# Kernel tuning notes

Hardware: AMD Instinct MI355X
Metric: run time of the kernel (lower is better)

## Reference

```python
import jax, jax.numpy as jnp
import numpy as np

N_NODES = 50000
N_EDGES = 800000
D = 128
N_LAYERS = 5
N_REL = 500
N_ENT = 50000  # fc output size (num_entities)
BATCH = 1024


def setup_inputs() -> dict:
    key = jax.random.key(0)
    ks = jax.random.split(key, 10)
    return {
        "entity_embed": jax.random.normal(ks[0], (N_NODES, D), dtype=jnp.float32),
        "edge_val": jnp.ones((N_EDGES,), dtype=jnp.float32),
        "gnn_W": jax.random.normal(ks[1], (N_LAYERS, D, D), dtype=jnp.float32) * (1.0 / np.sqrt(D)),
        "gnn_b": jax.random.normal(ks[2], (N_LAYERS, D), dtype=jnp.float32) * 0.01,
        "rel_table": jax.random.normal(ks[3], (N_REL, D), dtype=jnp.float32),
        "fc_W": jax.random.normal(ks[4], (2 * D, N_ENT), dtype=jnp.float32) * (1.0 / np.sqrt(2 * D)),
        "fc_b": jax.random.normal(ks[5], (N_ENT,), dtype=jnp.float32) * 0.01,
        "edge_row": jax.random.randint(ks[6], (N_EDGES,), 0, N_NODES, dtype=jnp.int32),
        "edge_col": jax.random.randint(ks[7], (N_EDGES,), 0, N_NODES, dtype=jnp.int32),
        "head_idx": jax.random.randint(ks[8], (BATCH,), 0, N_NODES, dtype=jnp.int32),
        "rel_ids": jax.random.randint(ks[9], (BATCH,), 0, N_REL, dtype=jnp.int32),
    }


def reference(entity_embed, edge_val, gnn_W, gnn_b, rel_table, fc_W, fc_b,
              edge_row, edge_col, head_idx, rel_ids):
    n_nodes = entity_embed.shape[0]

    def layer(x, wb):
        W, b = wb
        # sparse.mm(adj, x): out[row] += val * x[col]
        msgs = edge_val[:, None] * x[edge_col]          # [E, D]
        agg = jax.ops.segment_sum(msgs, edge_row, num_segments=n_nodes)  # [N, D]
        return jax.nn.relu(agg @ W + b), None

    all_embed, _ = jax.lax.scan(layer, entity_embed, (gnn_W, gnn_b))

    head_embed = all_embed[head_idx]                    # [B, D]
    rel_embed = rel_table[rel_ids]                      # [B, D]
    embed = jnp.concatenate([head_embed, rel_embed], axis=1)  # [B, 2D]
    logits = embed @ fc_W + fc_b                        # [B, N_ENT]
    return logits
```

## Files before the change

kernel.cpp:

```cpp
#include <hip/hip_runtime.h>


#define N_NODES 50000
#define N_EDGES 800000
#define D 128
#define N_LAYERS 5
#define N_ENT 50000
#define BATCH 1024
#define KDIM 256
#define SCAN_BLOCKS ((N_NODES + 255) / 256)
#define FC_NT 128

typedef __attribute__((ext_vector_type(8))) __bf16 bf16x8;
typedef __attribute__((ext_vector_type(4))) float f32x4;
typedef __attribute__((ext_vector_type(8))) unsigned short u16x8;
typedef __attribute__((ext_vector_type(4))) unsigned short u16x4;

__device__ inline unsigned short f2bf(float x) {
  unsigned int u = __float_as_uint(x);
  unsigned int r = (u + 0x7FFFu + ((u >> 16) & 1u)) >> 16;
  return (unsigned short)r;
}
__device__ inline float bf2f(unsigned short b) {
  return __uint_as_float(((unsigned int)b) << 16);
}

__global__ void zero_i32(int* __restrict__ p, int n) {
  int i = blockIdx.x * blockDim.x + threadIdx.x;
  if (i < n) p[i] = 0;
}

__global__ void hist_kernel(const int* __restrict__ rows, int* __restrict__ counts) {
  int i = blockIdx.x * blockDim.x + threadIdx.x;
  int stride = gridDim.x * blockDim.x;
  for (; i < N_EDGES; i += stride) atomicAdd(&counts[rows[i]], 1);
}

__device__ inline int block_exscan256(int v, int* wsum, int* tot) {
  int t = threadIdx.x, lane = t & 63, wid = t >> 6;
  int s = v;
#pragma unroll
  for (int off = 1; off < 64; off <<= 1) {
    int u = __shfl_up(s, off, 64);
    if (lane >= off) s += u;
  }
  if (lane == 63) wsum[wid] = s;
  __syncthreads();
  if (t == 0) {
    int run = 0;
#pragma unroll
    for (int w = 0; w < 4; ++w) { int tmp = wsum[w]; wsum[w] = run; run += tmp; }
    wsum[4] = run;
  }
  __syncthreads();
  *tot = wsum[4];
  return wsum[wid] + s - v;
}

__global__ __launch_bounds__(256) void scan1_kernel(const int* __restrict__ counts,
                                                    int* __restrict__ row_ptr,
                                                    int* __restrict__ bsum) {
  __shared__ int wsum[5];
  int i = blockIdx.x * 256 + threadIdx.x;
  int v = (i < N_NODES) ? counts[i] : 0;
  int tot;
  int ex = block_exscan256(v, wsum, &tot);
  if (i < N_NODES) row_ptr[i] = ex;
  if (threadIdx.x == 0) bsum[blockIdx.x] = tot;
}

__global__ __launch_bounds__(256) void scan2_kernel(int* __restrict__ bsum) {
  __shared__ int wsum[5];
  int t = threadIdx.x;
  int v = (t < SCAN_BLOCKS) ? bsum[t] : 0;
  int tot;
  int ex = block_exscan256(v, wsum, &tot);
  if (t < SCAN_BLOCKS) bsum[t] = ex;
}

__global__ __launch_bounds__(256) void scan3_kernel(const int* __restrict__ counts,
                                                    const int* __restrict__ bsum,
                                                    int* __restrict__ row_ptr,
                                                    int* __restrict__ cursor) {
  int i = blockIdx.x * 256 + threadIdx.x;
  if (i >= N_NODES) return;
  int ex = row_ptr[i] + bsum[blockIdx.x];
  row_ptr[i] = ex;
  cursor[i] = ex;
  if (i == N_NODES - 1) row_ptr[N_NODES] = ex + counts[i];
}

__global__ void scatter_kernel(const int* __restrict__ rows, const int* __restrict__ cols,
                               const float* __restrict__ vals, int* __restrict__ cursor,
                               int* __restrict__ col_s, float* __restrict__ val_s) {
  int i = blockIdx.x * blockDim.x + threadIdx.x;
  int stride = gridDim.x * blockDim.x;
  for (; i < N_EDGES; i += stride) {
    int r = rows[i];
    int pos = atomicAdd(&cursor[r], 1);
    col_s[pos] = cols[i];
    val_s[pos] = vals[i];
  }
}

__global__ __launch_bounds__(256) void tobf16_kernel(const float* __restrict__ src,
                                                     unsigned short* __restrict__ dst,
                                                     int n8) {
  int i = blockIdx.x * blockDim.x + threadIdx.x;
  if (i >= n8) return;
  float4 a = *(const float4*)&src[i * 8];
  float4 b = *(const float4*)&src[i * 8 + 4];
  u16x8 o;
  o[0] = f2bf(a.x); o[1] = f2bf(a.y); o[2] = f2bf(a.z); o[3] = f2bf(a.w);
  o[4] = f2bf(b.x); o[5] = f2bf(b.y); o[6] = f2bf(b.z); o[7] = f2bf(b.w);
  *(u16x8*)&dst[i * 8] = o;
}

__global__ void wconv_kernel(const float* __restrict__ gW, unsigned short* __restrict__ Wt5) {
  int idx = blockIdx.x * 256 + threadIdx.x;
  if (idx >= N_LAYERS * D * D) return;
  int l = idx / (D * D);
  int rem = idx - l * D * D;
  int j = rem >> 7;
  int k = rem & 127;
  Wt5[idx] = f2bf(gW[l * D * D + k * D + j]);
}

__global__ __launch_bounds__(256) void layer_fused(const unsigned short* __restrict__ xb,
                                                   const int* __restrict__ row_ptr,
                                                   const int* __restrict__ cols,
                                                   const float* __restrict__ vals,
                                                   const unsigned short* __restrict__ Bt,
                                                   const float* __restrict__ bias,
                                                   unsigned short* __restrict__ yb) {
  __shared__ unsigned short atile[64 * D];
  int t = threadIdx.x, lane = t & 63, wave = t >> 6;
  int q = lane >> 4, l16 = lane & 15;
  int r0 = blockIdx.x * 64;
  char* ab = (char*)atile;

#pragma unroll
  for (int p = 0; p < 4; ++p) {
    int row_l = wave * 16 + p * 4 + q;
    int r = r0 + row_l;
    float acc[8] = {0.f, 0.f, 0.f, 0.f, 0.f, 0.f, 0.f, 0.f};
    if (r < N_NODES) {
      int e0 = row_ptr[r], e1 = row_ptr[r + 1];
      for (int base = e0; base < e1; base += 16) {
        int idx = base + l16;
        bool ok = idx < e1;
        int cl = ok ? cols[idx] : 0;
        float vl = ok ? vals[idx] : 0.f;
        int cnt = min(16, e1 - base);
        int j = 0;
        for (; j + 4 <= cnt; j += 4) {
          int c[4]; float v[4]; u16x8 xv[4];
#pragma unroll
          for (int u = 0; u < 4; ++u) {
            c[u] = __shfl(cl, q * 16 + j + u);
            v[u] = __shfl(vl, q * 16 + j + u);
          }
#pragma unroll
          for (int u = 0; u < 4; ++u) xv[u] = *(const u16x8*)&xb[c[u] * D + l16 * 8];
#pragma unroll
          for (int u = 0; u < 4; ++u)
#pragma unroll
            for (int dd = 0; dd < 8; ++dd) acc[dd] = fmaf(v[u], bf2f(xv[u][dd]), acc[dd]);
        }
        for (; j < cnt; ++j) {
          int c = __shfl(cl, q * 16 + j);
          float v = __shfl(vl, q * 16 + j);
          u16x8 xv0 = *(const u16x8*)&xb[c * D + l16 * 8];
#pragma unroll
          for (int dd = 0; dd < 8; ++dd) acc[dd] = fmaf(v, bf2f(xv0[dd]), acc[dd]);
        }
      }
    }
    u16x8 o;
#pragma unroll
    for (int dd = 0; dd < 8; ++dd) o[dd] = f2bf(acc[dd]);
    *(u16x8*)(ab + row_l * 256 + ((l16 ^ (row_l & 7)) << 4)) = o;
  }
  __syncthreads();

  int lq = lane >> 4;
  f32x4 acc2[4][2];
#pragma unroll
  for (int m = 0; m < 4; ++m) { acc2[m][0] = (f32x4){0,0,0,0}; acc2[m][1] = (f32x4){0,0,0,0}; }
#pragma unroll
  for (int kk = 0; kk < 4; ++kk) {
    bf16x8 wfr[2];
#pragma unroll
    for (int nt = 0; nt < 2; ++nt)
      wfr[nt] = *(const bf16x8*)&Bt[(wave * 32 + nt * 16 + l16) * D + kk * 32 + lq * 8];
#pragma unroll
    for (int m = 0; m < 4; ++m) {
      int row_l = m * 16 + l16;
      bf16x8 afr = *(const bf16x8*)(ab + row_l * 256 + ((((kk * 4 + lq) ^ (row_l & 7)) << 4)));
      acc2[m][0] = __builtin_amdgcn_mfma_f32_16x16x32_bf16(wfr[0], afr, acc2[m][0], 0, 0, 0);
      acc2[m][1] = __builtin_amdgcn_mfma_f32_16x16x32_bf16(wfr[1], afr, acc2[m][1], 0, 0, 0);
    }
  }
#pragma unroll
  for (int nt = 0; nt < 2; ++nt) {
    int jb = wave * 32 + nt * 16 + lq * 4;
    float4 bb = *(const float4*)&bias[jb];
#pragma unroll
    for (int m = 0; m < 4; ++m) {
      int r = r0 + m * 16 + l16;
      if (r < N_NODES) {
        u16x4 o;
        o[0] = f2bf(fmaxf(acc2[m][nt][0] + bb.x, 0.f));
        o[1] = f2bf(fmaxf(acc2[m][nt][1] + bb.y, 0.f));
        o[2] = f2bf(fmaxf(acc2[m][nt][2] + bb.z, 0.f));
        o[3] = f2bf(fmaxf(acc2[m][nt][3] + bb.w, 0.f));
        *(u16x4*)&yb[(size_t)r * D + jb] = o;
      }
    }
  }
}

__global__ __launch_bounds__(256) void wt_kernel(const float* __restrict__ fcW,
                                                 unsigned short* __restrict__ Wt) {
  int n = blockIdx.x * 256 + threadIdx.x;
  int k0 = blockIdx.y * 8;
  if (n >= N_ENT) return;
  u16x8 pk;
#pragma unroll
  for (int e = 0; e < 8; ++e) pk[e] = f2bf(fcW[(size_t)(k0 + e) * N_ENT + n]);
  *(u16x8*)&Wt[(size_t)n * KDIM + k0] = pk;
}

__global__ __launch_bounds__(256) void gather_bf16(const unsigned short* __restrict__ xb,
                                                   const float* __restrict__ rel_table,
                                                   const int* __restrict__ head_idx,
                                                   const int* __restrict__ rel_ids,
                                                   unsigned short* __restrict__ ebf) {
  int b = blockIdx.x;
  int k = threadIdx.x;
  unsigned short v;
  if (k < D) v = xb[head_idx[b] * D + k];
  else       v = f2bf(rel_table[rel_ids[b] * D + (k - D)]);
  ebf[b * KDIM + k] = v;
}

__global__ __launch_bounds__(256, 2) void fc_mfma(const unsigned short* __restrict__ ebf,
                                                  const unsigned short* __restrict__ Wt,
                                                  const float* __restrict__ fcb,
                                                  float* __restrict__ out) {
  __shared__ unsigned short etile[64 * KDIM];
  int t = threadIdx.x;
  int lane = t & 63, wave = t >> 6;
  int l16 = lane & 15, lq = lane >> 4;
  int n0 = blockIdx.x * FC_NT;
  char* eb = (char*)etile;

  bf16x8 afr[2][8];
#pragma unroll
  for (int nt = 0; nt < 2; ++nt) {
    const unsigned short* wp = Wt + (size_t)(n0 + wave * 32 + nt * 16 + l16) * KDIM + lq * 8;
#pragma unroll
    for (int kk = 0; kk < 8; ++kk) afr[nt][kk] = *(const bf16x8*)(wp + kk * 32);
  }

  int n_st[2]; float4 bv[2];
#pragma unroll
  for (int nt = 0; nt < 2; ++nt) {
    n_st[nt] = n0 + wave * 32 + nt * 16 + lq * 4;
    bv[nt] = make_float4(0.f, 0.f, 0.f, 0.f);
    if (n_st[nt] < N_ENT) bv[nt] = *(const float4*)&fcb[n_st[nt]];
  }

  for (int bc = 0; bc < 8; ++bc) {
    int b0 = blockIdx.y * 512 + bc * 64;
    const char* esrc = (const char*)(ebf + (size_t)b0 * KDIM);
#pragma unroll
    for (int it = 0; it < 8; ++it) {
      int c = it * 256 + t;
      int row = c >> 5;
      int ci = c & 31;
      float4 v = *(const float4*)(esrc + (size_t)c * 16);
      *(float4*)(eb + row * 512 + ((ci ^ ((row & 7) << 2)) << 4)) = v;
    }
    __syncthreads();

    f32x4 acc[2][4];
#pragma unroll
    for (int nt = 0; nt < 2; ++nt)
#pragma unroll
      for (int m = 0; m < 4; ++m) acc[nt][m] = (f32x4){0.f, 0.f, 0.f, 0.f};

#pragma unroll
    for (int m = 0; m < 4; ++m) {
      int row = m * 16 + l16;
#pragma unroll
      for (int kk = 0; kk < 8; ++kk) {
        bf16x8 bfr = *(const bf16x8*)(eb + row * 512 + ((((kk * 4 + lq) ^ ((row & 7) << 2)) << 4)));
        acc[0][m] = __builtin_amdgcn_mfma_f32_16x16x32_bf16(afr[0][kk], bfr, acc[0][m], 0, 0, 0);
        acc[1][m] = __builtin_amdgcn_mfma_f32_16x16x32_bf16(afr[1][kk], bfr, acc[1][m], 0, 0, 0);
      }
    }

#pragma unroll
    for (int nt = 0; nt < 2; ++nt) {
      if (n_st[nt] < N_ENT) {
#pragma unroll
        for (int m = 0; m < 4; ++m) {
          int b = b0 + m * 16 + l16;
          float4 o = {acc[nt][m][0] + bv[nt].x, acc[nt][m][1] + bv[nt].y,
                      acc[nt][m][2] + bv[nt].z, acc[nt][m][3] + bv[nt].w};
          *(float4*)&out[(size_t)b * N_ENT + n_st[nt]] = o;
        }
      }
    }
    __syncthreads();
  }
}

extern "C" void kernel_launch(void* const* d_in, const int* in_sizes, int n_in,
                              void* d_out, int out_size, void* d_ws, size_t ws_size,
                              hipStream_t stream) {
  const float* entity    = (const float*)d_in[0];
  const float* edge_val  = (const float*)d_in[1];
  const float* gnn_W     = (const float*)d_in[2];
  const float* gnn_b     = (const float*)d_in[3];
  const float* rel_table = (const float*)d_in[4];
  const float* fc_W      = (const float*)d_in[5];
  const float* fc_b      = (const float*)d_in[6];
  const int* edge_row    = (const int*)d_in[7];
  const int* edge_col    = (const int*)d_in[8];
  const int* head_idx    = (const int*)d_in[9];
  const int* rel_ids     = (const int*)d_in[10];
  float* out = (float*)d_out;

  char* ws = (char*)d_ws;
  size_t off = 0;
  auto alloc = [&](size_t bytes) -> void* {
    void* p = ws + off;
    off = (off + bytes + 255) & ~(size_t)255;
    return p;
  };
  int* counts   = (int*)alloc((size_t)N_NODES * 4);
  int* row_ptr  = (int*)alloc((size_t)(N_NODES + 1) * 4);
  int* cursor   = (int*)alloc((size_t)N_NODES * 4);
  int* bsum     = (int*)alloc((size_t)256 * 4);
  int* col_s    = (int*)alloc((size_t)N_EDGES * 4);
  float* val_s  = (float*)alloc((size_t)N_EDGES * 4);
  unsigned short* xA    = (unsigned short*)alloc((size_t)N_NODES * D * 2);
  unsigned short* xB    = (unsigned short*)alloc((size_t)N_NODES * D * 2);
  unsigned short* entbf = (unsigned short*)alloc((size_t)N_NODES * D * 2);
  unsigned short* ebf   = (unsigned short*)alloc((size_t)BATCH * KDIM * 2);
  unsigned short* Wt    = (unsigned short*)alloc((size_t)(N_ENT + 256) * KDIM * 2);
  unsigned short* Wt5   = (unsigned short*)alloc((size_t)N_LAYERS * D * D * 2);

  zero_i32<<<(N_NODES + 255) / 256, 256, 0, stream>>>(counts, N_NODES);
  hist_kernel<<<1024, 256, 0, stream>>>(edge_row, counts);
  scan1_kernel<<<SCAN_BLOCKS, 256, 0, stream>>>(counts, row_ptr, bsum);
  scan2_kernel<<<1, 256, 0, stream>>>(bsum);
  scan3_kernel<<<SCAN_BLOCKS, 256, 0, stream>>>(counts, bsum, row_ptr, cursor);
  scatter_kernel<<<1024, 256, 0, stream>>>(edge_row, edge_col, edge_val, cursor, col_s, val_s);

  tobf16_kernel<<<(N_NODES * D / 8 + 255) / 256, 256, 0, stream>>>(entity, entbf, N_NODES * D / 8);
  wconv_kernel<<<(N_LAYERS * D * D + 255) / 256, 256, 0, stream>>>(gnn_W, Wt5);

  for (int layer = 0; layer < N_LAYERS; ++layer) {
    const unsigned short* xin = (layer == 0) ? entbf : ((layer & 1) ? xA : xB);
    unsigned short* yout = (layer & 1) ? xB : xA;
    layer_fused<<<(N_NODES + 63) / 64, 256, 0, stream>>>(xin, row_ptr, col_s, val_s,
                                                         Wt5 + (size_t)layer * D * D,
                                                         gnn_b + (size_t)layer * D, yout);
  }

  dim3 wtg((N_ENT + 255) / 256, KDIM / 8);
  wt_kernel<<<wtg, 256, 0, stream>>>(fc_W, Wt);
  gather_bf16<<<BATCH, KDIM, 0, stream>>>(xA, rel_table, head_idx, rel_ids, ebf);

  dim3 fcg((N_ENT + FC_NT - 1) / FC_NT, 2);
  fc_mfma<<<fcg, 256, 0, stream>>>(ebf, Wt, fc_b, out);
}
```

Measured before the change: 401.2 us.

## Interleave CSR edges, prefetch two edge batches, halve GNN rows per block, split FC batch

Sorted edge column and value arrays are packed into one int2 array so each edge needs one load, and the first 32 edges of each row are fetched up front to hide load latency. The fused GNN layer kernel now processes 32 rows per block instead of 64, doubling the grid to raise parallelism at the cost of reloading weight fragments more often. The FC kernel grid doubles in the batch dimension, with each block handling 256 batch rows instead of 512, which adds more concurrent blocks but reloads the Wt fragments more times.

```diff
diff --git a/kernel.cpp b/kernel.cpp
--- a/kernel.cpp
+++ b/kernel.cpp
@@ -92,14 +92,14 @@
 
 __global__ void scatter_kernel(const int* __restrict__ rows, const int* __restrict__ cols,
                                const float* __restrict__ vals, int* __restrict__ cursor,
-                               int* __restrict__ col_s, float* __restrict__ val_s) {
+                               int2* __restrict__ edge_s) {
   int i = blockIdx.x * blockDim.x + threadIdx.x;
   int stride = gridDim.x * blockDim.x;
   for (; i < N_EDGES; i += stride) {
     int r = rows[i];
     int pos = atomicAdd(&cursor[r], 1);
-    col_s[pos] = cols[i];
-    val_s[pos] = vals[i];
+    int2 ev = {cols[i], __float_as_int(vals[i])};
+    edge_s[pos] = ev;
   }
 }
 
@@ -126,54 +126,65 @@
   Wt5[idx] = f2bf(gW[l * D * D + k * D + j]);
 }
 
+__device__ inline void agg_batch(int cl, float vl, int cnt, int q, int l16,
+                                 const unsigned short* __restrict__ xb, float* acc) {
+  int j = 0;
+  for (; j + 4 <= cnt; j += 4) {
+    int c[4]; float v[4]; u16x8 xv[4];
+#pragma unroll
+    for (int u = 0; u < 4; ++u) {
+      c[u] = __shfl(cl, q * 16 + j + u);
+      v[u] = __shfl(vl, q * 16 + j + u);
+    }
+#pragma unroll
+    for (int u = 0; u < 4; ++u) xv[u] = *(const u16x8*)&xb[c[u] * D + l16 * 8];
+#pragma unroll
+    for (int u = 0; u < 4; ++u)
+#pragma unroll
+      for (int dd = 0; dd < 8; ++dd) acc[dd] = fmaf(v[u], bf2f(xv[u][dd]), acc[dd]);
+  }
+  for (; j < cnt; ++j) {
+    int c = __shfl(cl, q * 16 + j);
+    float v = __shfl(vl, q * 16 + j);
+    u16x8 xv0 = *(const u16x8*)&xb[c * D + l16 * 8];
+#pragma unroll
+    for (int dd = 0; dd < 8; ++dd) acc[dd] = fmaf(v, bf2f(xv0[dd]), acc[dd]);
+  }
+}
+
 __global__ __launch_bounds__(256) void layer_fused(const unsigned short* __restrict__ xb,
                                                    const int* __restrict__ row_ptr,
-                                                   const int* __restrict__ cols,
-                                                   const float* __restrict__ vals,
+                                                   const int2* __restrict__ edge_s,
                                                    const unsigned short* __restrict__ Bt,
                                                    const float* __restrict__ bias,
                                                    unsigned short* __restrict__ yb) {
-  __shared__ unsigned short atile[64 * D];
+  __shared__ unsigned short atile[32 * D];
   int t = threadIdx.x, lane = t & 63, wave = t >> 6;
   int q = lane >> 4, l16 = lane & 15;
-  int r0 = blockIdx.x * 64;
+  int r0 = blockIdx.x * 32;
   char* ab = (char*)atile;
 
 #pragma unroll
-  for (int p = 0; p < 4; ++p) {
-    int row_l = wave * 16 + p * 4 + q;
+  for (int p = 0; p < 2; ++p) {
+    int row_l = wave * 8 + p * 4 + q;
     int r = r0 + row_l;
     float acc[8] = {0.f, 0.f, 0.f, 0.f, 0.f, 0.f, 0.f, 0.f};
     if (r < N_NODES) {
       int e0 = row_ptr[r], e1 = row_ptr[r + 1];
-      for (int base = e0; base < e1; base += 16) {
+      int deg = e1 - e0;
+      int i0 = e0 + l16, i1 = e0 + 16 + l16;
+      int2 ev0 = {0, 0}, ev1 = {0, 0};
+      if (i0 < e1) ev0 = edge_s[i0];
+      if (i1 < e1) ev1 = edge_s[i1];
+      int cl0 = ev0.x; float vl0 = __int_as_float(ev0.y);
+      int cl1 = ev1.x; float vl1 = __int_as_float(ev1.y);
+      agg_batch(cl0, vl0, min(16, deg), q, l16, xb, acc);
+      if (deg > 16) agg_batch(cl1, vl1, min(16, deg - 16), q, l16, xb, acc);
+      for (int base = e0 + 32; base < e1; base += 16) {
         int idx = base + l16;
-        bool ok = idx < e1;
-        int cl = ok ? cols[idx] : 0;
-        float vl = ok ? vals[idx] : 0.f;
-        int cnt = min(16, e1 - base);
-        int j = 0;
-        for (; j + 4 <= cnt; j += 4) {
-          int c[4]; float v[4]; u16x8 xv[4];
-#pragma unroll
-          for (int u = 0; u < 4; ++u) {
-            c[u] = __shfl(cl, q * 16 + j + u);
-            v[u] = __shfl(vl, q * 16 + j + u);
-          }
-#pragma unroll
-          for (int u = 0; u < 4; ++u) xv[u] = *(const u16x8*)&xb[c[u] * D + l16 * 8];
-#pragma unroll
-          for (int u = 0; u < 4; ++u)
-#pragma unroll
-            for (int dd = 0; dd < 8; ++dd) acc[dd] = fmaf(v[u], bf2f(xv[u][dd]), acc[dd]);
-        }
-        for (; j < cnt; ++j) {
-          int c = __shfl(cl, q * 16 + j);
-          float v = __shfl(vl, q * 16 + j);
-          u16x8 xv0 = *(const u16x8*)&xb[c * D + l16 * 8];
-#pragma unroll
-          for (int dd = 0; dd < 8; ++dd) acc[dd] = fmaf(v, bf2f(xv0[dd]), acc[dd]);
-        }
+        int2 ev = {0, 0};
+        if (idx < e1) ev = edge_s[idx];
+        agg_batch(ev.x, __int_as_float(ev.y), min(16, e1 - base), q, l16, xb, acc);
       }
     }
     u16x8 o;
@@ -184,9 +195,9 @@
   __syncthreads();
 
   int lq = lane >> 4;
-  f32x4 acc2[4][2];
-#pragma unroll
-  for (int m = 0; m < 4; ++m) { acc2[m][0] = (f32x4){0,0,0,0}; acc2[m][1] = (f32x4){0,0,0,0}; }
+  f32x4 acc2[2][2];
+#pragma unroll
+  for (int m = 0; m < 2; ++m) { acc2[m][0] = (f32x4){0,0,0,0}; acc2[m][1] = (f32x4){0,0,0,0}; }
 #pragma unroll
   for (int kk = 0; kk < 4; ++kk) {
     bf16x8 wfr[2];
@@ -194,7 +205,7 @@
     for (int nt = 0; nt < 2; ++nt)
       wfr[nt] = *(const bf16x8*)&Bt[(wave * 32 + nt * 16 + l16) * D + kk * 32 + lq * 8];
 #pragma unroll
-    for (int m = 0; m < 4; ++m) {
+    for (int m = 0; m < 2; ++m) {
       int row_l = m * 16 + l16;
       bf16x8 afr = *(const bf16x8*)(ab + row_l * 256 + ((((kk * 4 + lq) ^ (row_l & 7)) << 4)));
       acc2[m][0] = __builtin_amdgcn_mfma_f32_16x16x32_bf16(wfr[0], afr, acc2[m][0], 0, 0, 0);
@@ -206,7 +217,7 @@
     int jb = wave * 32 + nt * 16 + lq * 4;
     float4 bb = *(const float4*)&bias[jb];
 #pragma unroll
-    for (int m = 0; m < 4; ++m) {
+    for (int m = 0; m < 2; ++m) {
       int r = r0 + m * 16 + l16;
       if (r < N_NODES) {
         u16x4 o;
@@ -271,8 +282,8 @@
     if (n_st[nt] < N_ENT) bv[nt] = *(const float4*)&fcb[n_st[nt]];
   }
 
-  for (int bc = 0; bc < 8; ++bc) {
-    int b0 = blockIdx.y * 512 + bc * 64;
+  for (int bc = 0; bc < 4; ++bc) {
+    int b0 = blockIdx.y * 256 + bc * 64;
     const char* esrc = (const char*)(ebf + (size_t)b0 * KDIM);
 #pragma unroll
     for (int it = 0; it < 8; ++it) {
@@ -344,8 +355,7 @@
   int* row_ptr  = (int*)alloc((size_t)(N_NODES + 1) * 4);
   int* cursor   = (int*)alloc((size_t)N_NODES * 4);
   int* bsum     = (int*)alloc((size_t)256 * 4);
-  int* col_s    = (int*)alloc((size_t)N_EDGES * 4);
-  float* val_s  = (float*)alloc((size_t)N_EDGES * 4);
+  int2* edge_s  = (int2*)alloc((size_t)N_EDGES * 8);
   unsigned short* xA    = (unsigned short*)alloc((size_t)N_NODES * D * 2);
   unsigned short* xB    = (unsigned short*)alloc((size_t)N_NODES * D * 2);
   unsigned short* entbf = (unsigned short*)alloc((size_t)N_NODES * D * 2);
@@ -358,7 +368,7 @@
   scan1_kernel<<<SCAN_BLOCKS, 256, 0, stream>>>(counts, row_ptr, bsum);
   scan2_kernel<<<1, 256, 0, stream>>>(bsum);
   scan3_kernel<<<SCAN_BLOCKS, 256, 0, stream>>>(counts, bsum, row_ptr, cursor);
-  scatter_kernel<<<1024, 256, 0, stream>>>(edge_row, edge_col, edge_val, cursor, col_s, val_s);
+  scatter_kernel<<<1024, 256, 0, stream>>>(edge_row, edge_col, edge_val, cursor, edge_s);
 
   tobf16_kernel<<<(N_NODES * D / 8 + 255) / 256, 256, 0, stream>>>(entity, entbf, N_NODES * D / 8);
   wconv_kernel<<<(N_LAYERS * D * D + 255) / 256, 256, 0, stream>>>(gnn_W, Wt5);
@@ -366,7 +376,7 @@
   for (int layer = 0; layer < N_LAYERS; ++layer) {
     const unsigned short* xin = (layer == 0) ? entbf : ((layer & 1) ? xA : xB);
     unsigned short* yout = (layer & 1) ? xB : xA;
-    layer_fused<<<(N_NODES + 63) / 64, 256, 0, stream>>>(xin, row_ptr, col_s, val_s,
+    layer_fused<<<(N_NODES + 31) / 32, 256, 0, stream>>>(xin, row_ptr, edge_s,
                                                          Wt5 + (size_t)layer * D * D,
                                                          gnn_b + (size_t)layer * D, yout);
   }
@@ -375,6 +385,6 @@
   wt_kernel<<<wtg, 256, 0, stream>>>(fc_W, Wt);
   gather_bf16<<<BATCH, KDIM, 0, stream>>>(xA, rel_table, head_idx, rel_ids, ebf);
 
-  dim3 fcg((N_ENT + FC_NT - 1) / FC_NT, 2);
+  dim3 fcg((N_ENT + FC_NT - 1) / FC_NT, 4);
   fc_mfma<<<fcg, 256, 0, stream>>>(ebf, Wt, fc_b, out);
 }
```

Result: slower. 418.1 us (+4.2%).

## Interleave edge col/val and aggregate two rows per lane group concurrently

Applied to the files above, without the earlier changes.

Edges are now stored as packed int2 (column, value) pairs, so the aggregation reads one 8-byte load per edge instead of two separate arrays. The SpMM aggregation loop now handles two rows per 16-lane group at once. It preloads the first 32 edges of each row up front and issues fixed groups of 4 gathers, padding partial groups with zero-weight edges. The aim is to keep more independent gathers in flight and hide memory latency. The cost is higher register pressure and some redundant gathers of node 0 for padded entries.

```diff
diff --git a/kernel.cpp b/kernel.cpp
--- a/kernel.cpp
+++ b/kernel.cpp
@@ -92,14 +92,14 @@
 
 __global__ void scatter_kernel(const int* __restrict__ rows, const int* __restrict__ cols,
                                const float* __restrict__ vals, int* __restrict__ cursor,
-                               int* __restrict__ col_s, float* __restrict__ val_s) {
+                               int2* __restrict__ edge_s) {
   int i = blockIdx.x * blockDim.x + threadIdx.x;
   int stride = gridDim.x * blockDim.x;
   for (; i < N_EDGES; i += stride) {
     int r = rows[i];
     int pos = atomicAdd(&cursor[r], 1);
-    col_s[pos] = cols[i];
-    val_s[pos] = vals[i];
+    int2 ev = {cols[i], __float_as_int(vals[i])};
+    edge_s[pos] = ev;
   }
 }
 
@@ -126,10 +126,25 @@
   Wt5[idx] = f2bf(gW[l * D * D + k * D + j]);
 }
 
+__device__ inline void group4(int cl, float vl, int jbase, int q, int l16,
+                              const unsigned short* __restrict__ xb, float* acc) {
+  int c[4]; float v[4]; u16x8 xv[4];
+#pragma unroll
+  for (int u = 0; u < 4; ++u) {
+    c[u] = __shfl(cl, q * 16 + jbase + u);
+    v[u] = __shfl(vl, q * 16 + jbase + u);
+  }
+#pragma unroll
+  for (int u = 0; u < 4; ++u) xv[u] = *(const u16x8*)&xb[c[u] * D + l16 * 8];
+#pragma unroll
+  for (int u = 0; u < 4; ++u)
+#pragma unroll
+    for (int dd = 0; dd < 8; ++dd) acc[dd] = fmaf(v[u], bf2f(xv[u][dd]), acc[dd]);
+}
+
 __global__ __launch_bounds__(256) void layer_fused(const unsigned short* __restrict__ xb,
                                                    const int* __restrict__ row_ptr,
-                                                   const int* __restrict__ cols,
-                                                   const float* __restrict__ vals,
+                                                   const int2* __restrict__ edge_s,
                                                    const unsigned short* __restrict__ Bt,
                                                    const float* __restrict__ bias,
                                                    unsigned short* __restrict__ yb) {
@@ -140,46 +155,63 @@
   char* ab = (char*)atile;
 
 #pragma unroll
-  for (int p = 0; p < 4; ++p) {
-    int row_l = wave * 16 + p * 4 + q;
-    int r = r0 + row_l;
-    float acc[8] = {0.f, 0.f, 0.f, 0.f, 0.f, 0.f, 0.f, 0.f};
-    if (r < N_NODES) {
-      int e0 = row_ptr[r], e1 = row_ptr[r + 1];
-      for (int base = e0; base < e1; base += 16) {
-        int idx = base + l16;
-        bool ok = idx < e1;
-        int cl = ok ? cols[idx] : 0;
-        float vl = ok ? vals[idx] : 0.f;
-        int cnt = min(16, e1 - base);
-        int j = 0;
-        for (; j + 4 <= cnt; j += 4) {
-          int c[4]; float v[4]; u16x8 xv[4];
-#pragma unroll
-          for (int u = 0; u < 4; ++u) {
-            c[u] = __shfl(cl, q * 16 + j + u);
-            v[u] = __shfl(vl, q * 16 + j + u);
-          }
-#pragma unroll
-          for (int u = 0; u < 4; ++u) xv[u] = *(const u16x8*)&xb[c[u] * D + l16 * 8];
-#pragma unroll
-          for (int u = 0; u < 4; ++u)
-#pragma unroll
-            for (int dd = 0; dd < 8; ++dd) acc[dd] = fmaf(v[u], bf2f(xv[u][dd]), acc[dd]);
-        }
-        for (; j < cnt; ++j) {
-          int c = __shfl(cl, q * 16 + j);
-          float v = __shfl(vl, q * 16 + j);
-          u16x8 xv0 = *(const u16x8*)&xb[c * D + l16 * 8];
-#pragma unroll
-          for (int dd = 0; dd < 8; ++dd) acc[dd] = fmaf(v, bf2f(xv0[dd]), acc[dd]);
-        }
-      }
-    }
-    u16x8 o;
-#pragma unroll
-    for (int dd = 0; dd < 8; ++dd) o[dd] = f2bf(acc[dd]);
-    *(u16x8*)(ab + row_l * 256 + ((l16 ^ (row_l & 7)) << 4)) = o;
+  for (int p = 0; p < 2; ++p) {
+    int rowA = wave * 16 + p * 8 + q;
+    int rowB = rowA + 4;
+    int rA = r0 + rowA, rB = r0 + rowB;
+    float accA[8] = {0.f, 0.f, 0.f, 0.f, 0.f, 0.f, 0.f, 0.f};
+    float accB[8] = {0.f, 0.f, 0.f, 0.f, 0.f, 0.f, 0.f, 0.f};
+
+    int e0A = 0, e1A = 0, e0B = 0, e1B = 0;
+    if (rA < N_NODES) { e0A = row_ptr[rA]; e1A = row_ptr[rA + 1]; }
+    if (rB < N_NODES) { e0B = row_ptr[rB]; e1B = row_ptr[rB + 1]; }
+    int degA = e1A - e0A, degB = e1B - e0B;
+
+    int2 evA0 = {0, 0}, evA1 = {0, 0}, evB0 = {0, 0}, evB1 = {0, 0};
+    if (e0A + l16 < e1A)      evA0 = edge_s[e0A + l16];
+    if (e0A + 16 + l16 < e1A) evA1 = edge_s[e0A + 16 + l16];
+    if (e0B + l16 < e1B)      evB0 = edge_s[e0B + l16];
+    if (e0B + 16 + l16 < e1B) evB1 = edge_s[e0B + 16 + l16];
+    int clA0 = evA0.x; float vlA0 = __int_as_float(evA0.y);
+    int clA1 = evA1.x; float vlA1 = __int_as_float(evA1.y);
+    int clB0 = evB0.x; float vlB0 = __int_as_float(evB0.y);
+    int clB1 = evB1.x; float vlB1 = __int_as_float(evB1.y);
+
+#pragma unroll
+    for (int g = 0; g < 4; ++g) {
+      if (g * 4 < degA) group4(clA0, vlA0, g * 4, q, l16, xb, accA);
+      if (g * 4 < degB) group4(clB0, vlB0, g * 4, q, l16, xb, accB);
+    }
+    int dA1 = degA - 16, dB1 = degB - 16;
+#pragma unroll
+    for (int g = 0; g < 4; ++g) {
+      if (g * 4 < dA1) group4(clA1, vlA1, g * 4, q, l16, xb, accA);
+      if (g * 4 < dB1) group4(clB1, vlB1, g * 4, q, l16, xb, accB);
+    }
+    for (int base = e0A + 32; base < e1A; base += 16) {
+      int idx = base + l16;
+      int2 ev = {0, 0};
+      if (idx < e1A) ev = edge_s[idx];
+      int cnt = e1A - base;
+#pragma unroll
+      for (int g = 0; g < 4; ++g)
+        if (g * 4 < cnt) group4(ev.x, __int_as_float(ev.y), g * 4, q, l16, xb, accA);
+    }
+    for (int base = e0B + 32; base < e1B; base += 16) {
+      int idx = base + l16;
+      int2 ev = {0, 0};
+      if (idx < e1B) ev = edge_s[idx];
+      int cnt = e1B - base;
+#pragma unroll
+      for (int g = 0; g < 4; ++g)
+        if (g * 4 < cnt) group4(ev.x, __int_as_float(ev.y), g * 4, q, l16, xb, accB);
+    }
+
+    u16x8 oA, oB;
+#pragma unroll
+    for (int dd = 0; dd < 8; ++dd) { oA[dd] = f2bf(accA[dd]); oB[dd] = f2bf(accB[dd]); }
+    *(u16x8*)(ab + rowA * 256 + ((l16 ^ (rowA & 7)) << 4)) = oA;
+    *(u16x8*)(ab + rowB * 256 + ((l16 ^ (rowB & 7)) << 4)) = oB;
   }
   __syncthreads();
 
@@ -344,8 +376,7 @@
   int* row_ptr  = (int*)alloc((size_t)(N_NODES + 1) * 4);
   int* cursor   = (int*)alloc((size_t)N_NODES * 4);
   int* bsum     = (int*)alloc((size_t)256 * 4);
-  int* col_s    = (int*)alloc((size_t)N_EDGES * 4);
-  float* val_s  = (float*)alloc((size_t)N_EDGES * 4);
+  int2* edge_s  = (int2*)alloc((size_t)N_EDGES * 8);
   unsigned short* xA    = (unsigned short*)alloc((size_t)N_NODES * D * 2);
   unsigned short* xB    = (unsigned short*)alloc((size_t)N_NODES * D * 2);
   unsigned short* entbf = (unsigned short*)alloc((size_t)N_NODES * D * 2);
@@ -358,7 +389,7 @@
   scan1_kernel<<<SCAN_BLOCKS, 256, 0, stream>>>(counts, row_ptr, bsum);
   scan2_kernel<<<1, 256, 0, stream>>>(bsum);
   scan3_kernel<<<SCAN_BLOCKS, 256, 0, stream>>>(counts, bsum, row_ptr, cursor);
-  scatter_kernel<<<1024, 256, 0, stream>>>(edge_row, edge_col, edge_val, cursor, col_s, val_s);
+  scatter_kernel<<<1024, 256, 0, stream>>>(edge_row, edge_col, edge_val, cursor, edge_s);
 
   tobf16_kernel<<<(N_NODES * D / 8 + 255) / 256, 256, 0, stream>>>(entity, entbf, N_NODES * D / 8);
   wconv_kernel<<<(N_LAYERS * D * D + 255) / 256, 256, 0, stream>>>(gnn_W, Wt5);
@@ -366,7 +397,7 @@
   for (int layer = 0; layer < N_LAYERS; ++layer) {
     const unsigned short* xin = (layer == 0) ? entbf : ((layer & 1) ? xA : xB);
     unsigned short* yout = (layer & 1) ? xB : xA;
-    layer_fused<<<(N_NODES + 63) / 64, 256, 0, stream>>>(xin, row_ptr, col_s, val_s,
+    layer_fused<<<(N_NODES + 63) / 64, 256, 0, stream>>>(xin, row_ptr, edge_s,
                                                          Wt5 + (size_t)layer * D * D,
                                                          gnn_b + (size_t)layer * D, yout);
   }
```

Measured after the change: 428.4 us. 6.8% more time.

## Pre-pack FC activations in MFMA fragment layout and drop LDS staging

Applied to the files above, without the earlier changes.

The gather kernel now writes the batch embeddings directly in the per-lane MFMA B-fragment order, vectorized with 8 elements per thread. The FC kernel loads those fragments straight from global memory (L2-resident), which removes the shared-memory tile, its swizzled stores and both barriers. It processes 16 batch rows per iteration with fewer accumulators, and the occupancy hint of 2 is dropped. Every block now re-reads the packed activations from global or L2 instead of LDS. The aggregation loop is also factored into a helper, a refactor with no speed intent.

```diff
diff --git a/kernel.cpp b/kernel.cpp
--- a/kernel.cpp
+++ b/kernel.cpp
@@ -124,6 +124,32 @@
   int j = rem >> 7;
   int k = rem & 127;
   Wt5[idx] = f2bf(gW[l * D * D + k * D + j]);
+}
+
+__device__ inline void agg_batch(int cl, float vl, int cnt, int q, int l16,
+                                 const unsigned short* __restrict__ xb, float* acc) {
+  int j = 0;
+  for (; j + 4 <= cnt; j += 4) {
+    int c[4]; float v[4]; u16x8 xv[4];
+#pragma unroll
+    for (int u = 0; u < 4; ++u) {
+      c[u] = __shfl(cl, q * 16 + j + u);
+      v[u] = __shfl(vl, q * 16 + j + u);
+    }
+#pragma unroll
+    for (int u = 0; u < 4; ++u) xv[u] = *(const u16x8*)&xb[c[u] * D + l16 * 8];
+#pragma unroll
+    for (int u = 0; u < 4; ++u)
+#pragma unroll
+      for (int dd = 0; dd < 8; ++dd) acc[dd] = fmaf(v[u], bf2f(xv[u][dd]), acc[dd]);
+  }
+  for (; j < cnt; ++j) {
+    int c = __shfl(cl, q * 16 + j);
+    float v = __shfl(vl, q * 16 + j);
+    u16x8 xv0 = *(const u16x8*)&xb[c * D + l16 * 8];
+#pragma unroll
+    for (int dd = 0; dd < 8; ++dd) acc[dd] = fmaf(v, bf2f(xv0[dd]), acc[dd]);
+  }
 }
 
 __global__ __launch_bounds__(256) void layer_fused(const unsigned short* __restrict__ xb,
@@ -151,29 +177,7 @@
         bool ok = idx < e1;
         int cl = ok ? cols[idx] : 0;
         float vl = ok ? vals[idx] : 0.f;
-        int cnt = min(16, e1 - base);
-        int j = 0;
-        for (; j + 4 <= cnt; j += 4) {
-          int c[4]; float v[4]; u16x8 xv[4];
-#pragma unroll
-          for (int u = 0; u < 4; ++u) {
-            c[u] = __shfl(cl, q * 16 + j + u);
-            v[u] = __shfl(vl, q * 16 + j + u);
-          }
-#pragma unroll
-          for (int u = 0; u < 4; ++u) xv[u] = *(const u16x8*)&xb[c[u] * D + l16 * 8];
-#pragma unroll
-          for (int u = 0; u < 4; ++u)
-#pragma unroll
-            for (int dd = 0; dd < 8; ++dd) acc[dd] = fmaf(v[u], bf2f(xv[u][dd]), acc[dd]);
-        }
-        for (; j < cnt; ++j) {
-          int c = __shfl(cl, q * 16 + j);
-          float v = __shfl(vl, q * 16 + j);
-          u16x8 xv0 = *(const u16x8*)&xb[c * D + l16 * 8];
-#pragma unroll
-          for (int dd = 0; dd < 8; ++dd) acc[dd] = fmaf(v, bf2f(xv0[dd]), acc[dd]);
-        }
+        agg_batch(cl, vl, min(16, e1 - base), q, l16, xb, acc);
       }
     }
     u16x8 o;
@@ -231,29 +235,39 @@
   *(u16x8*)&Wt[(size_t)n * KDIM + k0] = pk;
 }
 
-__global__ __launch_bounds__(256) void gather_bf16(const unsigned short* __restrict__ xb,
+__global__ __launch_bounds__(256) void gather_pack(const unsigned short* __restrict__ xb,
                                                    const float* __restrict__ rel_table,
                                                    const int* __restrict__ head_idx,
                                                    const int* __restrict__ rel_ids,
-                                                   unsigned short* __restrict__ ebf) {
-  int b = blockIdx.x;
-  int k = threadIdx.x;
-  unsigned short v;
-  if (k < D) v = xb[head_idx[b] * D + k];
-  else       v = f2bf(rel_table[rel_ids[b] * D + (k - D)]);
-  ebf[b * KDIM + k] = v;
-}
-
-__global__ __launch_bounds__(256, 2) void fc_mfma(const unsigned short* __restrict__ ebf,
-                                                  const unsigned short* __restrict__ Wt,
-                                                  const float* __restrict__ fcb,
-                                                  float* __restrict__ out) {
-  __shared__ unsigned short etile[64 * KDIM];
+                                                   unsigned short* __restrict__ ebfP) {
+  int tid = blockIdx.x * 256 + threadIdx.x;
+  int b = tid >> 5;
+  int kl = tid & 31;
+  int kk = kl >> 2, lq = kl & 3;
+  int k0 = kk * 32 + lq * 8;
+  u16x8 v;
+  if (k0 < D) {
+    v = *(const u16x8*)&xb[head_idx[b] * D + k0];
+  } else {
+    const float* rp = &rel_table[rel_ids[b] * D + (k0 - D)];
+    float4 a = *(const float4*)rp;
+    float4 c = *(const float4*)(rp + 4);
+    v[0] = f2bf(a.x); v[1] = f2bf(a.y); v[2] = f2bf(a.z); v[3] = f2bf(a.w);
+    v[4] = f2bf(c.x); v[5] = f2bf(c.y); v[6] = f2bf(c.z); v[7] = f2bf(c.w);
+  }
+  int bchunk = b >> 4, l16 = b & 15;
+  int lane = lq * 16 + l16;
+  *(u16x8*)&ebfP[((size_t)(bchunk * 8 + kk) << 9) + lane * 8] = v;
+}
+
+__global__ __launch_bounds__(256) void fc_mfma(const unsigned short* __restrict__ ebfP,
+                                               const unsigned short* __restrict__ Wt,
+                                               const float* __restrict__ fcb,
+                                               float* __restrict__ out) {
   int t = threadIdx.x;
   int lane = t & 63, wave = t >> 6;
   int l16 = lane & 15, lq = lane >> 4;
   int n0 = blockIdx.x * FC_NT;
-  char* eb = (char*)etile;
 
   bf16x8 afr[2][8];
 #pragma unroll
@@ -271,49 +285,28 @@
     if (n_st[nt] < N_ENT) bv[nt] = *(const float4*)&fcb[n_st[nt]];
   }
 
-  for (int bc = 0; bc < 8; ++bc) {
-    int b0 = blockIdx.y * 512 + bc * 64;
-    const char* esrc = (const char*)(ebf + (size_t)b0 * KDIM);
-#pragma unroll
-    for (int it = 0; it < 8; ++it) {
-      int c = it * 256 + t;
-      int row = c >> 5;
-      int ci = c & 31;
-      float4 v = *(const float4*)(esrc + (size_t)c * 16);
-      *(float4*)(eb + row * 512 + ((ci ^ ((row & 7) << 2)) << 4)) = v;
-    }
-    __syncthreads();
-
-    f32x4 acc[2][4];
-#pragma unroll
-    for (int nt = 0; nt < 2; ++nt)
-#pragma unroll
-      for (int m = 0; m < 4; ++m) acc[nt][m] = (f32x4){0.f, 0.f, 0.f, 0.f};
-
-#pragma unroll
-    for (int m = 0; m < 4; ++m) {
-      int row = m * 16 + l16;
-#pragma unroll
-      for (int kk = 0; kk < 8; ++kk) {
-        bf16x8 bfr = *(const bf16x8*)(eb + row * 512 + ((((kk * 4 + lq) ^ ((row & 7) << 2)) << 4)));
-        acc[0][m] = __builtin_amdgcn_mfma_f32_16x16x32_bf16(afr[0][kk], bfr, acc[0][m], 0, 0, 0);
-        acc[1][m] = __builtin_amdgcn_mfma_f32_16x16x32_bf16(afr[1][kk], bfr, acc[1][m], 0, 0, 0);
-      }
-    }
-
-#pragma unroll
-    for (int nt = 0; nt < 2; ++nt) {
-      if (n_st[nt] < N_ENT) {
-#pragma unroll
-        for (int m = 0; m < 4; ++m) {
-          int b = b0 + m * 16 + l16;
-          float4 o = {acc[nt][m][0] + bv[nt].x, acc[nt][m][1] + bv[nt].y,
-                      acc[nt][m][2] + bv[nt].z, acc[nt][m][3] + bv[nt].w};
-          *(float4*)&out[(size_t)b * N_ENT + n_st[nt]] = o;
-        }
-      }
-    }
-    __syncthreads();
+  for (int c = 0; c < 32; ++c) {
+    int chunk = blockIdx.y * 32 + c;
+    const unsigned short* bp = ebfP + ((size_t)chunk * 8 << 9) + lane * 8;
+    bf16x8 bfr[8];
+#pragma unroll
+    for (int kk = 0; kk < 8; ++kk) bfr[kk] = *(const bf16x8*)(bp + (kk << 9));
+    f32x4 acc0 = (f32x4){0.f, 0.f, 0.f, 0.f};
+    f32x4 acc1 = (f32x4){0.f, 0.f, 0.f, 0.f};
+#pragma unroll
+    for (int kk = 0; kk < 8; ++kk) {
+      acc0 = __builtin_amdgcn_mfma_f32_16x16x32_bf16(afr[0][kk], bfr[kk], acc0, 0, 0, 0);
+      acc1 = __builtin_amdgcn_mfma_f32_16x16x32_bf16(afr[1][kk], bfr[kk], acc1, 0, 0, 0);
+    }
+    int b = chunk * 16 + l16;
+    if (n_st[0] < N_ENT) {
+      float4 o = {acc0[0] + bv[0].x, acc0[1] + bv[0].y, acc0[2] + bv[0].z, acc0[3] + bv[0].w};
+      *(float4*)&out[(size_t)b * N_ENT + n_st[0]] = o;
+    }
+    if (n_st[1] < N_ENT) {
+      float4 o = {acc1[0] + bv[1].x, acc1[1] + bv[1].y, acc1[2] + bv[1].z, acc1[3] + bv[1].w};
+      *(float4*)&out[(size_t)b * N_ENT + n_st[1]] = o;
+    }
   }
 }
 
@@ -349,7 +342,7 @@
   unsigned short* xA    = (unsigned short*)alloc((size_t)N_NODES * D * 2);
   unsigned short* xB    = (unsigned short*)alloc((size_t)N_NODES * D * 2);
   unsigned short* entbf = (unsigned short*)alloc((size_t)N_NODES * D * 2);
-  unsigned short* ebf   = (unsigned short*)alloc((size_t)BATCH * KDIM * 2);
+  unsigned short* ebfP  = (unsigned short*)alloc((size_t)BATCH * KDIM * 2);
   unsigned short* Wt    = (unsigned short*)alloc((size_t)(N_ENT + 256) * KDIM * 2);
   unsigned short* Wt5   = (unsigned short*)alloc((size_t)N_LAYERS * D * D * 2);
 
@@ -373,8 +366,8 @@
 
   dim3 wtg((N_ENT + 255) / 256, KDIM / 8);
   wt_kernel<<<wtg, 256, 0, stream>>>(fc_W, Wt);
-  gather_bf16<<<BATCH, KDIM, 0, stream>>>(xA, rel_table, head_idx, rel_ids, ebf);
+  gather_pack<<<BATCH * 32 / 256, 256, 0, stream>>>(xA, rel_table, head_idx, rel_ids, ebfP);
 
   dim3 fcg((N_ENT + FC_NT - 1) / FC_NT, 2);
-  fc_mfma<<<fcg, 256, 0, stream>>>(ebf, Wt, fc_b, out);
-}
+  fc_mfma<<<fcg, 256, 0, stream>>>(ebfP, Wt, fc_b, out);
+}
```

Measured after the change: 429.0 us. 1.07x slower.
